# Kernel optimization log

Measured on AMD Instinct MI355X. Metric: run time of the kernel, lower is better.

The kernel has to match this reference:

```python
import jax, jax.numpy as jnp
import numpy as np

H = 32          # hidden_size
NUM_LAYERS = 3
B, T, IN = 16384, 64, 2


def _gru_dir(x, Wih, Whh, bih, bhh, reverse):
    """Single-direction GRU over x:[B,T,I] with PyTorch gate math."""
    # Precompute input projections for all timesteps: [B,T,3H]
    xg = jnp.einsum('bti,gi->btg', x, Wih) + bih
    if reverse:
        xg = xg[:, ::-1]

    def step(h, xt):
        gh = h @ Whh.T + bhh                      # [B,3H]
        xr, xz, xn = jnp.split(xt, 3, axis=-1)
        hr, hz, hn = jnp.split(gh, 3, axis=-1)
        r = jax.nn.sigmoid(xr + hr)
        z = jax.nn.sigmoid(xz + hz)
        n = jnp.tanh(xn + r * hn)
        h2 = (1.0 - z) * n + z * h
        return h2, h2

    h0 = jnp.zeros((x.shape[0], H), x.dtype)
    _, hs = jax.lax.scan(step, h0, jnp.swapaxes(xg, 0, 1))  # [T,B,H]
    hs = jnp.swapaxes(hs, 0, 1)                              # [B,T,H]
    if reverse:
        hs = hs[:, ::-1]
    return hs


def setup_inputs() -> dict:
    key = jax.random.key(0)
    ks = jax.random.split(key, 11)
    s = 0.2  # weight scale ~ uniform(-1/sqrt(H)) magnitude
    return {
        'x':    jax.random.normal(ks[0], (B, T, IN), jnp.float32),
        'Wih0': jax.random.normal(ks[1], (2, 3 * H, IN), jnp.float32) * s,
        'Whh0': jax.random.normal(ks[2], (2, 3 * H, H), jnp.float32) * s,
        'bih0': jax.random.normal(ks[3], (2, 3 * H), jnp.float32) * s,
        'bhh0': jax.random.normal(ks[4], (2, 3 * H), jnp.float32) * s,
        'Wih':  jax.random.normal(ks[5], (NUM_LAYERS - 1, 2, 3 * H, 2 * H), jnp.float32) * s,
        'Whh':  jax.random.normal(ks[6], (NUM_LAYERS - 1, 2, 3 * H, H), jnp.float32) * s,
        'bih':  jax.random.normal(ks[7], (NUM_LAYERS - 1, 2, 3 * H), jnp.float32) * s,
        'bhh':  jax.random.normal(ks[8], (NUM_LAYERS - 1, 2, 3 * H), jnp.float32) * s,
        'Wfc':  jax.random.normal(ks[9], (2, 2 * H), jnp.float32) * s,
        'bfc':  jax.random.normal(ks[10], (2,), jnp.float32) * s,
    }


def reference(x, Wih0, Whh0, bih0, bhh0, Wih, Whh, bih, bhh, Wfc, bfc):
    out = x
    for l in range(NUM_LAYERS):
        if l == 0:
            wi, wh, bi, bh = Wih0, Whh0, bih0, bhh0
        else:
            wi, wh, bi, bh = Wih[l - 1], Whh[l - 1], bih[l - 1], bhh[l - 1]
        fwd = _gru_dir(out, wi[0], wh[0], bi[0], bh[0], reverse=False)
        bwd = _gru_dir(out, wi[1], wh[1], bi[1], bh[1], reverse=True)
        out = jnp.concatenate([fwd, bwd], axis=-1)  # [B,T,2H]
    y = out @ Wfc.T + bfc                            # [B,T,2]
    return jnp.tanh(y)
```

## Files before the change

kernel.cpp:

```cpp
#include <hip/hip_runtime.h>
#include <cstdint>
#include <cstddef>


#define BB 16384
#define TT 64
#define PS ((size_t)BB * 32)
#define DS ((size_t)TT * PS)
#define PT ((size_t)TT * BB * 2)

typedef __attribute__((ext_vector_type(8))) _Float16 f16x8;
typedef __attribute__((ext_vector_type(4))) float f32x4;
typedef __attribute__((ext_vector_type(2))) float f32x2;

#if __has_builtin(__builtin_amdgcn_exp2f)
#define EXP2(x) __builtin_amdgcn_exp2f(x)
#else
#define EXP2(x) exp2f(x)
#endif
#if __has_builtin(__builtin_amdgcn_rcpf)
#define RCP(x) __builtin_amdgcn_rcpf(x)
#else
#define RCP(x) (1.0f / (x))
#endif

#define SR (-1.4426950408889634f)
#define SN (-2.8853900817779268f)

__device__ __forceinline__ f32x2 mk2(float a, float b) {
    f32x2 v; v.x = a; v.y = b; return v;
}
__device__ __forceinline__ float tanh_fast(float x) { return 2.0f / (1.0f + __expf(-2.0f * x)) - 1.0f; }
__device__ __forceinline__ unsigned short f2h(float f) {
    _Float16 h = (_Float16)f;
    return __builtin_bit_cast(unsigned short, h);
}
__device__ __forceinline__ unsigned int cvt_pkh(float a, float b) {
#if __has_builtin(__builtin_amdgcn_cvt_pkrtz)
    typedef __fp16 h2_t __attribute__((ext_vector_type(2)));
    h2_t p = __builtin_amdgcn_cvt_pkrtz(a, b);
    return __builtin_bit_cast(unsigned int, p);
#else
    return (unsigned int)f2h(a) | ((unsigned int)f2h(b) << 16);
#endif
}
__device__ __forceinline__ f32x4 mfma16h(f16x8 a, f16x8 b, f32x4 c) {
    return __builtin_amdgcn_mfma_f32_16x16x32_f16(a, b, c, 0, 0, 0);
}

__device__ __forceinline__ void gate_pair2(f32x2 aR, f32x2 aZ, f32x2 xN, f32x2 hN,
                                           f32x2& hp) {
    f32x2 er = mk2(EXP2(aR.x), EXP2(aR.y));
    f32x2 ez = mk2(EXP2(aZ.x), EXP2(aZ.y));
    f32x2 Ar = er + 1.f;
    f32x2 Az = ez + 1.f;
    float iR = RCP(Ar.x * Ar.y);
    float iZ = RCP(Az.x * Az.y);
    f32x2 r = mk2(iR * Ar.y, iR * Ar.x);
    f32x2 z = mk2(iZ * Az.y, iZ * Az.x);
    f32x2 v = r * hN + xN;
    f32x2 en = mk2(EXP2(v.x), EXP2(v.y));
    f32x2 An = en + 1.f;
    float iN = RCP(An.x * An.y);
    f32x2 n = mk2(fmaf(2.f, iN * An.y, -1.f), fmaf(2.f, iN * An.x, -1.f));
    hp = z * (hp - n) + n;
}


template<bool IS_L0, bool IS_LAST>
__global__ __launch_bounds__(256, 2)
void gru_mfma(const float* __restrict__ x0,
              const unsigned short* __restrict__ bin,
              const float* __restrict__ Wih,
              const float* __restrict__ Whh,
              const float* __restrict__ bih,
              const float* __restrict__ bhh,
              unsigned short* __restrict__ bout,
              const float* __restrict__ Wfc,
              float* __restrict__ pbase)
{
    const int tid  = threadIdx.x;
    const int lane = tid & 63;
    const int wv   = tid >> 6;
    const int g    = blockIdx.x * 4 + wv;
    const int d    = g >> 10;
    const int b0   = (g & 1023) * 16;
    const int col  = lane & 15;
    const int qd   = lane >> 4;

    f16x8 whhF[6];
    {
        const float* wsrc = Whh + d * 96 * 32;
        #pragma unroll
        for (int t = 0; t < 6; ++t) {
            const float sc = (t < 4) ? SR : SN;
            const int row = (t >> 1) * 32 + 8 * (col >> 2) + 4 * (t & 1) + (col & 3);
            const float* pr = wsrc + row * 32 + qd * 8;
            unsigned short wbits[8];
            #pragma unroll
            for (int j = 0; j < 8; ++j) wbits[j] = f2h(pr[j] * sc);
            whhF[t] = __builtin_bit_cast(f16x8, *(uint4*)wbits);
        }
    }

    f16x8 wihF[6][2];
    float w0c[6][4], w1c[6][4];
    if constexpr (!IS_L0) {
        const float* wsrc = Wih + d * 96 * 64;
        #pragma unroll
        for (int t = 0; t < 6; ++t) {
            const float sc = (t < 4) ? SR : SN;
            const int row = (t >> 1) * 32 + 8 * (col >> 2) + 4 * (t & 1) + (col & 3);
            #pragma unroll
            for (int kc = 0; kc < 2; ++kc) {
                const float* pr = wsrc + row * 64 + kc * 32 + qd * 8;
                unsigned short wbits[8];
                #pragma unroll
                for (int j = 0; j < 8; ++j) wbits[j] = f2h(pr[j] * sc);
                wihF[t][kc] = __builtin_bit_cast(f16x8, *(uint4*)wbits);
            }
        }
    } else {
        #pragma unroll
        for (int t = 0; t < 6; ++t) {
            const float sc = (t < 4) ? SR : SN;
            #pragma unroll
            for (int q = 0; q < 4; ++q) {
                const int row = (t >> 1) * 32 + 8 * qd + 4 * (t & 1) + q;
                const float* pr = Wih + d * 96 * 2 + row * 2;
                w0c[t][q] = pr[0] * sc;
                w1c[t][q] = pr[1] * sc;
            }
        }
    }

    f32x4 biasIn[6], biasHN[2];
    {
        const float* bi = bih + d * 96;
        const float* bh = bhh + d * 96;
        #pragma unroll
        for (int t = 0; t < 4; ++t) {
            const int off = (t >> 1) * 32 + 8 * qd + 4 * (t & 1);
            float4 a = *(const float4*)(bi + off);
            float4 b = *(const float4*)(bh + off);
            biasIn[t][0] = (a.x + b.x) * SR; biasIn[t][1] = (a.y + b.y) * SR;
            biasIn[t][2] = (a.z + b.z) * SR; biasIn[t][3] = (a.w + b.w) * SR;
        }
        #pragma unroll
        for (int T = 0; T < 2; ++T) {
            const int off = 64 + 8 * qd + 4 * T;
            float4 a = *(const float4*)(bi + off);
            float4 b = *(const float4*)(bh + off);
            biasIn[4 + T][0] = a.x * SN; biasIn[4 + T][1] = a.y * SN;
            biasIn[4 + T][2] = a.z * SN; biasIn[4 + T][3] = a.w * SN;
            biasHN[T][0] = b.x * SN; biasHN[T][1] = b.y * SN;
            biasHN[T][2] = b.z * SN; biasHN[T][3] = b.w * SN;
        }
    }

    float wf0[2][4], wf1[2][4];
    if constexpr (IS_LAST) {
        #pragma unroll
        for (int T = 0; T < 2; ++T)
            #pragma unroll
            for (int q = 0; q < 4; ++q) {
                const int u = 8 * qd + 4 * T + q;
                wf0[T][q] = Wfc[d * 32 + u];
                wf1[T][q] = Wfc[64 + d * 32 + u];
            }
    }

    const int t0 = d ? (TT - 1) : 0;
    const int dt = d ? -1 : 1;
    const ptrdiff_t dplane = (ptrdiff_t)dt * (ptrdiff_t)PS;

    f16x8 hF = {};
    float hprev[2][4] = {{0.f,0.f,0.f,0.f},{0.f,0.f,0.f,0.f}};

    auto REC = [&](f32x4 (&acc)[6], f32x4 (&accHN)[2]) {
        #pragma unroll
        for (int t = 0; t < 4; ++t)
            acc[t] = mfma16h(whhF[t], hF, acc[t]);
        #pragma unroll
        for (int T = 0; T < 2; ++T)
            accHN[T] = mfma16h(whhF[4 + T], hF, biasHN[T]);
    };

    auto PROJ = [&](f32x4 (&accN)[6], uint4 nx0, uint4 nx1, float2 nxs) {
        if constexpr (!IS_L0) {
            f16x8 a0 = __builtin_bit_cast(f16x8, nx0);
            f16x8 a1 = __builtin_bit_cast(f16x8, nx1);
            #pragma unroll
            for (int t = 0; t < 6; ++t) {
                accN[t] = mfma16h(wihF[t][0], a0, biasIn[t]);
                accN[t] = mfma16h(wihF[t][1], a1, accN[t]);
            }
        } else {
            #pragma unroll
            for (int t = 0; t < 6; ++t)
                #pragma unroll
                for (int q = 0; q < 4; ++q)
                    accN[t][q] = fmaf(nxs.x, w0c[t][q], fmaf(nxs.y, w1c[t][q], biasIn[t][q]));
        }
    };

    auto GATES = [&](f32x4 (&acc)[6], f32x4 (&accHN)[2], unsigned short* outp,
                     uint4& hwP, unsigned short*& opP, float* poutp) {
        unsigned int hw[4];
        #pragma unroll
        for (int T = 0; T < 2; ++T) {
            f32x2 hp01 = mk2(hprev[T][0], hprev[T][1]);
            f32x2 hp23 = mk2(hprev[T][2], hprev[T][3]);
            gate_pair2(mk2(acc[T][0], acc[T][1]), mk2(acc[2 + T][0], acc[2 + T][1]),
                       mk2(acc[4 + T][0], acc[4 + T][1]), mk2(accHN[T][0], accHN[T][1]), hp01);
            gate_pair2(mk2(acc[T][2], acc[T][3]), mk2(acc[2 + T][2], acc[2 + T][3]),
                       mk2(acc[4 + T][2], acc[4 + T][3]), mk2(accHN[T][2], accHN[T][3]), hp23);
            hprev[T][0] = hp01.x; hprev[T][1] = hp01.y;
            hprev[T][2] = hp23.x; hprev[T][3] = hp23.y;
            hw[2 * T]     = cvt_pkh(hp01.x, hp01.y);
            hw[2 * T + 1] = cvt_pkh(hp23.x, hp23.y);
        }
        hF = __builtin_bit_cast(f16x8, *(uint4*)hw);
        if constexpr (IS_LAST) {
            float p0 = 0.f, p1 = 0.f;
            #pragma unroll
            for (int T = 0; T < 2; ++T)
                #pragma unroll
                for (int q = 0; q < 4; ++q) {
                    p0 = fmaf(hprev[T][q], wf0[T][q], p0);
                    p1 = fmaf(hprev[T][q], wf1[T][q], p1);
                }
            p0 += __shfl_xor(p0, 16); p0 += __shfl_xor(p0, 32);
            p1 += __shfl_xor(p1, 16); p1 += __shfl_xor(p1, 32);
            if (qd == 0) *(float2*)poutp = make_float2(p0, p1);
        } else {
            *(uint4*)opP = hwP;
            hwP = *(uint4*)hw;
            opP = outp;
        }
    };

    f32x4 accA[6], accB[6], accHN[2];
    uint4 xc0 = {}, xc1 = {}, xe0 = {}, xe1 = {};
    float2 xsc = {}, xse = {};
    const unsigned short* xFE = nullptr; const unsigned short* xBE = nullptr;
    const unsigned short* xFO = nullptr; const unsigned short* xBO = nullptr;
    const float* xfpE = nullptr; const float* xfpO = nullptr;

    if constexpr (!IS_L0) {
        const unsigned short* pF = bin + (size_t)t0 * PS + (size_t)(b0 + col) * 32 + qd * 8;
        const unsigned short* pB = pF + DS;
        uint4 a = *(const uint4*)pF, b = *(const uint4*)pB;
        PROJ(accA, a, b, {});
        xc0 = *(const uint4*)(pF + dplane);
        xc1 = *(const uint4*)(pB + dplane);
        xFE = pF + 2 * dplane; xBE = pB + 2 * dplane;
        xFO = pF + 3 * dplane; xBO = pB + 3 * dplane;
    } else {
        const float* p0 = x0 + ((size_t)(b0 + col) * TT + t0) * 2;
        float2 xs0 = *(const float2*)p0;
        PROJ(accA, {}, {}, xs0);
        xsc = *(const float2*)(p0 + dt * 2);
        xfpE = p0 + dt * 4;
        xfpO = p0 + dt * 6;
    }

    unsigned short* optrA = nullptr; unsigned short* optrB = nullptr;
    float* poutA = nullptr; float* poutB = nullptr;
    const ptrdiff_t dpp = (ptrdiff_t)dt * (ptrdiff_t)BB * 2;
    if constexpr (IS_LAST) {
        poutA = pbase + (size_t)d * PT + ((size_t)t0 * BB + b0 + col) * 2;
        poutB = poutA + dpp;
    } else {
        optrA = bout + (size_t)d * DS + (size_t)t0 * PS + (size_t)(b0 + col) * 32 + qd * 8;
        optrB = optrA + dplane;
    }

    uint4 hwPrevA = {}, hwPrevB = {};
    unsigned short* opPrevA = optrA;
    unsigned short* opPrevB = optrB;

    for (int k = 0; k < 31; ++k) {
        if constexpr (!IS_L0) {
            xe0 = *(const uint4*)xFE; xe1 = *(const uint4*)xBE;
            xFE += 2 * dplane; xBE += 2 * dplane;
        } else { xse = *(const float2*)xfpE; xfpE += dt * 4; }
        REC(accA, accHN);
        PROJ(accB, xc0, xc1, xsc);
        GATES(accA, accHN, optrA, hwPrevA, opPrevA, poutA);
        if constexpr (IS_LAST) poutA += 2 * dpp; else optrA += 2 * dplane;
        if constexpr (!IS_L0) {
            xc0 = *(const uint4*)xFO; xc1 = *(const uint4*)xBO;
            xFO += 2 * dplane; xBO += 2 * dplane;
        } else { xsc = *(const float2*)xfpO; xfpO += dt * 4; }
        REC(accB, accHN);
        PROJ(accA, xe0, xe1, xse);
        GATES(accB, accHN, optrB, hwPrevB, opPrevB, poutB);
        if constexpr (IS_LAST) poutB += 2 * dpp; else optrB += 2 * dplane;
    }
    REC(accA, accHN);
    PROJ(accB, xc0, xc1, xsc);
    GATES(accA, accHN, optrA, hwPrevA, opPrevA, poutA);
    REC(accB, accHN);
    GATES(accB, accHN, optrB, hwPrevB, opPrevB, poutB);
    if constexpr (!IS_LAST) {
        *(uint4*)opPrevA = hwPrevA;
        *(uint4*)opPrevB = hwPrevB;
    }
}

__global__ __launch_bounds__(256)
void fc_finish(const float* __restrict__ pf,
               const float* __restrict__ pb,
               const float* __restrict__ bfc,
               float* __restrict__ out)
{
    __shared__ float2 tile[64][65];
    const int tid = threadIdx.x;
    const int bbase = blockIdx.x * 64;
    const float c0 = bfc[0], c1 = bfc[1];
    #pragma unroll
    for (int tp = 0; tp < 16; ++tp) {
        const int t = tp * 4 + (tid >> 6);
        const int bl = tid & 63;
        const size_t idx = ((size_t)t * BB + bbase + bl) * 2;
        float2 vf = *(const float2*)(pf + idx);
        float2 vb = *(const float2*)(pb + idx);
        float2 o;
        o.x = tanh_fast(vf.x + vb.x + c0);
        o.y = tanh_fast(vf.y + vb.y + c1);
        tile[t][bl] = o;
    }
    __syncthreads();
    #pragma unroll
    for (int bp = 0; bp < 16; ++bp) {
        const int bl = bp * 4 + (tid >> 6);
        const int t = tid & 63;
        *(float2*)(out + ((size_t)(bbase + bl) * TT + t) * 2) = tile[t][bl];
    }
}

extern "C" void kernel_launch(void* const* d_in, const int* in_sizes, int n_in,
                              void* d_out, int out_size, void* d_ws, size_t ws_size,
                              hipStream_t stream)
{
    const float* x    = (const float*)d_in[0];
    const float* Wih0 = (const float*)d_in[1];
    const float* Whh0 = (const float*)d_in[2];
    const float* bih0 = (const float*)d_in[3];
    const float* bhh0 = (const float*)d_in[4];
    const float* WihL = (const float*)d_in[5];
    const float* WhhL = (const float*)d_in[6];
    const float* bihL = (const float*)d_in[7];
    const float* bhhL = (const float*)d_in[8];
    const float* Wfc  = (const float*)d_in[9];
    const float* bfc  = (const float*)d_in[10];

    unsigned short* buf0 = (unsigned short*)d_ws;
    unsigned short* buf1 = buf0 + 2 * DS;
    float* pbase = (float*)d_ws;
    float* out = (float*)d_out;

    gru_mfma<true, false><<<512, 256, 0, stream>>>(
        x, nullptr, Wih0, Whh0, bih0, bhh0, buf0, nullptr, nullptr);
    gru_mfma<false, false><<<512, 256, 0, stream>>>(
        nullptr, buf0, WihL, WhhL, bihL, bhhL, buf1, nullptr, nullptr);
    gru_mfma<false, true><<<512, 256, 0, stream>>>(
        nullptr, buf1, WihL + 2 * 96 * 64, WhhL + 2 * 96 * 32,
        bihL + 2 * 96, bhhL + 2 * 96, nullptr, Wfc, pbase);
    fc_finish<<<BB / 64, 256, 0, stream>>>(
        pbase, pbase + PT, bfc, out);
}
```

Measured before the change: 267.8 us.

## Split each GRU batch tile's hidden units across two waves exchanging state via LDS

Adds a new gru_split kernel for the first two layers. Each 16-sequence tile is handled by a 128-thread block whose two waves each own half of the hidden units, and they exchange half-hidden-state through double-buffered shared memory with a barrier every timestep. This shortens the per-wave serial gate chain and raises the number of resident waves (2048 blocks), in exchange for a __syncthreads and an LDS round trip per step. The last layer still uses the original kernel.

Result: slower. 285.4 us (+6.6%).

```diff
diff --git a/kernel.cpp b/kernel.cpp
--- a/kernel.cpp
+++ b/kernel.cpp
@@ -66,6 +66,209 @@
     hp = z * (hp - n) + n;
 }
 
+
+template<bool IS_L0>
+__global__ __launch_bounds__(128, 4)
+void gru_split(const float* __restrict__ x0,
+               const unsigned short* __restrict__ bin,
+               const float* __restrict__ Wih,
+               const float* __restrict__ Whh,
+               const float* __restrict__ bih,
+               const float* __restrict__ bhh,
+               unsigned short* __restrict__ bout)
+{
+    __shared__ uint2 xch[2][2][64];
+
+    const int tid  = threadIdx.x;
+    const int lane = tid & 63;
+    const int w    = tid >> 6;
+    const int g    = blockIdx.x;
+    const int d    = g >> 10;
+    const int b0   = (g & 1023) * 16;
+    const int col  = lane & 15;
+    const int qd   = lane >> 4;
+
+    f16x8 whhF[3];
+    {
+        const float* wsrc = Whh + d * 96 * 32;
+        #pragma unroll
+        for (int gg = 0; gg < 3; ++gg) {
+            const float sc = (gg < 2) ? SR : SN;
+            const int row = gg * 32 + 8 * (col >> 2) + 4 * w + (col & 3);
+            const float* pr = wsrc + row * 32 + qd * 8;
+            unsigned short wbits[8];
+            #pragma unroll
+            for (int j = 0; j < 8; ++j) wbits[j] = f2h(pr[j] * sc);
+            whhF[gg] = __builtin_bit_cast(f16x8, *(uint4*)wbits);
+        }
+    }
+
+    f16x8 wihF[3][2];
+    float w0c[3][4], w1c[3][4];
+    if constexpr (!IS_L0) {
+        const float* wsrc = Wih + d * 96 * 64;
+        #pragma unroll
+        for (int gg = 0; gg < 3; ++gg) {
+            const float sc = (gg < 2) ? SR : SN;
+            const int row = gg * 32 + 8 * (col >> 2) + 4 * w + (col & 3);
+            #pragma unroll
+            for (int kc = 0; kc < 2; ++kc) {
+                const float* pr = wsrc + row * 64 + kc * 32 + qd * 8;
+                unsigned short wbits[8];
+                #pragma unroll
+                for (int j = 0; j < 8; ++j) wbits[j] = f2h(pr[j] * sc);
+                wihF[gg][kc] = __builtin_bit_cast(f16x8, *(uint4*)wbits);
+            }
+        }
+    } else {
+        #pragma unroll
+        for (int gg = 0; gg < 3; ++gg) {
+            const float sc = (gg < 2) ? SR : SN;
+            #pragma unroll
+            for (int q = 0; q < 4; ++q) {
+                const int row = gg * 32 + 8 * qd + 4 * w + q;
+                const float* pr = Wih + d * 96 * 2 + row * 2;
+                w0c[gg][q] = pr[0] * sc;
+                w1c[gg][q] = pr[1] * sc;
+            }
+        }
+    }
+
+    f32x4 biasIn[3], biasHN;
+    {
+        const float* bi = bih + d * 96;
+        const float* bh = bhh + d * 96;
+        #pragma unroll
+        for (int gg = 0; gg < 2; ++gg) {
+            const int off = gg * 32 + 8 * qd + 4 * w;
+            float4 a = *(const float4*)(bi + off);
+            float4 b = *(const float4*)(bh + off);
+            biasIn[gg][0] = (a.x + b.x) * SR; biasIn[gg][1] = (a.y + b.y) * SR;
+            biasIn[gg][2] = (a.z + b.z) * SR; biasIn[gg][3] = (a.w + b.w) * SR;
+        }
+        const int off = 64 + 8 * qd + 4 * w;
+        float4 a = *(const float4*)(bi + off);
+        float4 b = *(const float4*)(bh + off);
+        biasIn[2][0] = a.x * SN; biasIn[2][1] = a.y * SN;
+        biasIn[2][2] = a.z * SN; biasIn[2][3] = a.w * SN;
+        biasHN[0] = b.x * SN; biasHN[1] = b.y * SN;
+        biasHN[2] = b.z * SN; biasHN[3] = b.w * SN;
+    }
+
+    const int t0 = d ? (TT - 1) : 0;
+    const int dt = d ? -1 : 1;
+    const ptrdiff_t dplane = (ptrdiff_t)dt * (ptrdiff_t)PS;
+
+    f16x8 hF = {};
+    float hprev[4] = {0.f, 0.f, 0.f, 0.f};
+    uint2 hwOwn = {0u, 0u};
+    f32x4 accA[3], accB[3], accHN;
+
+    auto REC = [&](f32x4 (&acc)[3]) {
+        acc[0] = mfma16h(whhF[0], hF, acc[0]);
+        acc[1] = mfma16h(whhF[1], hF, acc[1]);
+        accHN  = mfma16h(whhF[2], hF, biasHN);
+    };
+
+    auto PROJ = [&](f32x4 (&acc)[3], uint4 nx0, uint4 nx1, float2 nxs) {
+        if constexpr (!IS_L0) {
+            f16x8 a0 = __builtin_bit_cast(f16x8, nx0);
+            f16x8 a1 = __builtin_bit_cast(f16x8, nx1);
+            #pragma unroll
+            for (int gg = 0; gg < 3; ++gg) {
+                acc[gg] = mfma16h(wihF[gg][0], a0, biasIn[gg]);
+                acc[gg] = mfma16h(wihF[gg][1], a1, acc[gg]);
+            }
+        } else {
+            #pragma unroll
+            for (int gg = 0; gg < 3; ++gg)
+                #pragma unroll
+                for (int q = 0; q < 4; ++q)
+                    acc[gg][q] = fmaf(nxs.x, w0c[gg][q], fmaf(nxs.y, w1c[gg][q], biasIn[gg][q]));
+        }
+    };
+
+    auto GATES = [&](f32x4 (&acc)[3]) {
+        f32x2 hp01 = mk2(hprev[0], hprev[1]);
+        f32x2 hp23 = mk2(hprev[2], hprev[3]);
+        gate_pair2(mk2(acc[0][0], acc[0][1]), mk2(acc[1][0], acc[1][1]),
+                   mk2(acc[2][0], acc[2][1]), mk2(accHN[0], accHN[1]), hp01);
+        gate_pair2(mk2(acc[0][2], acc[0][3]), mk2(acc[1][2], acc[1][3]),
+                   mk2(acc[2][2], acc[2][3]), mk2(accHN[2], accHN[3]), hp23);
+        hprev[0] = hp01.x; hprev[1] = hp01.y;
+        hprev[2] = hp23.x; hprev[3] = hp23.y;
+        hwOwn.x = cvt_pkh(hp01.x, hp01.y);
+        hwOwn.y = cvt_pkh(hp23.x, hp23.y);
+    };
+
+    const unsigned short* pF = nullptr; const unsigned short* pB = nullptr;
+    const float* pfx = nullptr;
+    unsigned short* optr = bout + (size_t)d * DS + (size_t)t0 * PS
+                         + (size_t)(b0 + col) * 32 + 8 * qd + 4 * w;
+
+    if constexpr (!IS_L0) {
+        const unsigned short* laneF = bin + (size_t)t0 * PS + (size_t)(b0 + col) * 32 + qd * 8;
+        const unsigned short* laneB = laneF + DS;
+        uint4 a = *(const uint4*)laneF, b = *(const uint4*)laneB;
+        PROJ(accA, a, b, {});
+        a = *(const uint4*)(laneF + dplane); b = *(const uint4*)(laneB + dplane);
+        accHN = biasHN;
+        GATES(accA);
+        xch[0][w][lane] = hwOwn;
+        *(uint2*)optr = hwOwn; optr += dplane;
+        PROJ(accB, a, b, {});
+        pF = laneF + 2 * dplane; pB = laneB + 2 * dplane;
+    } else {
+        const float* lane0 = x0 + ((size_t)(b0 + col) * TT + t0) * 2;
+        float2 xs0 = *(const float2*)lane0;
+        float2 xs1 = *(const float2*)(lane0 + dt * 2);
+        PROJ(accA, {}, {}, xs0);
+        accHN = biasHN;
+        GATES(accA);
+        xch[0][w][lane] = hwOwn;
+        *(uint2*)optr = hwOwn; optr += dplane;
+        PROJ(accB, {}, {}, xs1);
+        pfx = lane0 + dt * 4;
+    }
+
+    auto STEP = [&](f32x4 (&accCur)[3], f32x4 (&accNext)[3], int pCons) {
+        __syncthreads();
+        uint4 xn0 = {}, xn1 = {}; float2 xns = {};
+        if constexpr (!IS_L0) {
+            xn0 = *(const uint4*)pF; xn1 = *(const uint4*)pB;
+            pF += dplane; pB += dplane;
+        } else {
+            xns = *(const float2*)pfx; pfx += dt * 2;
+        }
+        uint2 oth = xch[pCons][1 - w][lane];
+        uint4 hv;
+        if (w == 0) { hv.x = hwOwn.x; hv.y = hwOwn.y; hv.z = oth.x; hv.w = oth.y; }
+        else        { hv.x = oth.x;   hv.y = oth.y;   hv.z = hwOwn.x; hv.w = hwOwn.y; }
+        hF = __builtin_bit_cast(f16x8, hv);
+        REC(accCur);
+        GATES(accCur);
+        xch[1 - pCons][w][lane] = hwOwn;
+        *(uint2*)optr = hwOwn; optr += dplane;
+        PROJ(accNext, xn0, xn1, xns);
+    };
+
+    for (int k = 0; k < 31; ++k) {
+        STEP(accB, accA, 0);
+        STEP(accA, accB, 1);
+    }
+
+    __syncthreads();
+    {
+        uint2 oth = xch[0][1 - w][lane];
+        uint4 hv;
+        if (w == 0) { hv.x = hwOwn.x; hv.y = hwOwn.y; hv.z = oth.x; hv.w = oth.y; }
+        else        { hv.x = oth.x;   hv.y = oth.y;   hv.z = hwOwn.x; hv.w = hwOwn.y; }
+        hF = __builtin_bit_cast(f16x8, hv);
+        REC(accB);
+        GATES(accB);
+        *(uint2*)optr = hwOwn;
+    }
+}
 
 template<bool IS_L0, bool IS_LAST>
 __global__ __launch_bounds__(256, 2)
@@ -361,10 +564,10 @@
     float* pbase = (float*)d_ws;
     float* out = (float*)d_out;
 
-    gru_mfma<true, false><<<512, 256, 0, stream>>>(
-        x, nullptr, Wih0, Whh0, bih0, bhh0, buf0, nullptr, nullptr);
-    gru_mfma<false, false><<<512, 256, 0, stream>>>(
-        nullptr, buf0, WihL, WhhL, bihL, bhhL, buf1, nullptr, nullptr);
+    gru_split<true><<<2048, 128, 0, stream>>>(
+        x, nullptr, Wih0, Whh0, bih0, bhh0, buf0);
+    gru_split<false><<<2048, 128, 0, stream>>>(
+        nullptr, buf0, WihL, WhhL, bihL, bhhL, buf1);
     gru_mfma<false, true><<<512, 256, 0, stream>>>(
         nullptr, buf1, WihL + 2 * 96 * 64, WhhL + 2 * 96 * 32,
         bihL + 2 * 96, bhhL + 2 * 96, nullptr, Wfc, pbase);
```
